# Kernel optimization log

Measured on AMD Instinct MI355X. Metric: run time of the kernel, lower is better.

Reference implementation:

```python
import jax, jax.numpy as jnp
import numpy as np

B, D = 8192, 1024
HR, HE, HF = 512, 4096, 2048
N_OPS, N_TASKS = 4, 4

def setup_inputs() -> dict:
    key = jax.random.key(0)
    ks = jax.random.split(key, 20)
    s = 0.02
    return {
        "x":        jax.random.normal(ks[0], (B, D), jnp.float32),
        # router
        "W_r1":   s*jax.random.normal(ks[1], (D, HR), jnp.float32),
        "b_r1":     jnp.zeros((HR,), jnp.float32),
        "W_dom":  s*jax.random.normal(ks[2], (HR, 2), jnp.float32),
        "b_dom":    jnp.zeros((2,), jnp.float32),
        "W_mop":  s*jax.random.normal(ks[3], (HR, N_OPS), jnp.float32),
        "W_lt":   s*jax.random.normal(ks[4], (HR, N_TASKS), jnp.float32),
        # math expert (operation hint = additive embedding)
        "op_emb": s*jax.random.normal(ks[5], (N_OPS, D), jnp.float32),
        "W_m1":   s*jax.random.normal(ks[6], (D, HE), jnp.float32),
        "b_m1":     jnp.zeros((HE,), jnp.float32),
        "W_m2":   s*jax.random.normal(ks[7], (HE, D), jnp.float32),
        "b_m2":     jnp.zeros((D,), jnp.float32),
        # language expert (task hint = additive embedding)
        "task_emb": s*jax.random.normal(ks[8], (N_TASKS, D), jnp.float32),
        "W_l1":   s*jax.random.normal(ks[9], (D, HE), jnp.float32),
        "b_l1":     jnp.zeros((HE,), jnp.float32),
        "W_l2":   s*jax.random.normal(ks[10], (HE, D), jnp.float32),
        "b_l2":     jnp.zeros((D,), jnp.float32),
        # fusion
        "W_f1":   s*jax.random.normal(ks[11], (D, HF), jnp.float32),
        "b_f1":     jnp.zeros((HF,), jnp.float32),
        "W_f2":   s*jax.random.normal(ks[12], (HF, D), jnp.float32),
        "b_f2":     jnp.zeros((D,), jnp.float32),
    }

def reference(x, W_r1, b_r1, W_dom, b_dom, W_mop, W_lt,
              op_emb, W_m1, b_m1, W_m2, b_m2,
              task_emb, W_l1, b_l1, W_l2, b_l2,
              W_f1, b_f1, W_f2, b_f2):
    # --- router ---
    h = jax.nn.relu(x @ W_r1 + b_r1)                      # [B, HR]
    dom_logits = h @ W_dom + b_dom                        # [B, 2]
    expert_weights = jax.nn.softmax(dom_logits, axis=-1)  # [B, 2]
    primary = jnp.argmax(dom_logits, axis=-1)             # [B]
    math_op = jnp.argmax(h @ W_mop, axis=-1)              # [B]
    lang_task = jnp.argmax(h @ W_lt, axis=-1)             # [B]
    # --- experts (vectorized equivalent of per-sample dispatch) ---
    math_in = x + op_emb[math_op]                         # [B, D]
    math_out = jax.nn.relu(math_in @ W_m1 + b_m1) @ W_m2 + b_m2
    lang_in = x + task_emb[lang_task]                     # [B, D]
    lang_out = jax.nn.relu(lang_in @ W_l1 + b_l1) @ W_l2 + b_l2
    selected = jnp.where((primary == 0)[:, None], math_out, lang_out)  # [B, D]
    # --- fusion: scale by routing weight of the chosen expert + MLP residual ---
    w = jnp.take_along_axis(expert_weights, primary[:, None], axis=1)  # [B, 1]
    fused = w * selected
    final = fused + jax.nn.relu(fused @ W_f1 + b_f1) @ W_f2 + b_f2     # [B, D]
    return final
```

## Files before the change

kernel.cpp:

```cpp
#include <hip/hip_runtime.h>
#include <hip/hip_bf16.h>
#include <stdint.h>

#define NB 8192
#define DD 1024
#define HRD 512
#define HED 4096
#define HFD 2048

typedef __attribute__((ext_vector_type(8))) short bf16x8;
typedef __attribute__((ext_vector_type(4))) float f32x4;
typedef unsigned short u16;

__device__ __forceinline__ u16 f2b(float f) {
    union { float f; uint32_t i; } c; c.f = f;
    uint32_t r = c.i + 0x7FFF + ((c.i >> 16) & 1);
    return (u16)(r >> 16);
}
__device__ __forceinline__ float b2f(u16 u) {
    union { uint32_t i; float f; } c; c.i = ((uint32_t)u) << 16; return c.f;
}

__global__ void k_init(int* cnt) { if (threadIdx.x < 2) cnt[threadIdx.x] = 0; }

__global__ __launch_bounds__(256) void k_split(const float4* __restrict__ x4,
                                               ushort4* __restrict__ hi4,
                                               ushort4* __restrict__ lo4) {
    int i = blockIdx.x * 256 + threadIdx.x;
    float4 v = x4[i];
    ushort4 h, l;
    h.x = f2b(v.x); l.x = f2b(v.x - b2f(h.x));
    h.y = f2b(v.y); l.y = f2b(v.y - b2f(h.y));
    h.z = f2b(v.z); l.z = f2b(v.z - b2f(h.z));
    h.w = f2b(v.w); l.w = f2b(v.w - b2f(h.w));
    hi4[i] = h; lo4[i] = l;
}

__global__ __launch_bounds__(256) void k_transpose(const float* __restrict__ in,
                                                   u16* __restrict__ out, int R, int C) {
    __shared__ float s[64][65];
    int tx = threadIdx.x & 63, ty = threadIdx.x >> 6;
    int c0 = blockIdx.x * 64, r0 = blockIdx.y * 64;
#pragma unroll
    for (int j = 0; j < 16; j++) { int r = ty + j * 4; s[r][tx] = in[(size_t)(r0 + r) * C + c0 + tx]; }
    __syncthreads();
#pragma unroll
    for (int j = 0; j < 16; j++) { int c = ty + j * 4; out[(size_t)(c0 + c) * R + r0 + tx] = f2b(s[tx][c]); }
}

__global__ __launch_bounds__(256) void k_transpose_split(const float* __restrict__ in,
                                                         u16* __restrict__ ohi, u16* __restrict__ olo,
                                                         int R, int C) {
    __shared__ float s[64][65];
    int tx = threadIdx.x & 63, ty = threadIdx.x >> 6;
    int c0 = blockIdx.x * 64, r0 = blockIdx.y * 64;
#pragma unroll
    for (int j = 0; j < 16; j++) { int r = ty + j * 4; s[r][tx] = in[(size_t)(r0 + r) * C + c0 + tx]; }
    __syncthreads();
#pragma unroll
    for (int j = 0; j < 16; j++) {
        int c = ty + j * 4;
        float v = s[tx][c];
        u16 h = f2b(v);
        ohi[(size_t)(c0 + c) * R + r0 + tx] = h;
        olo[(size_t)(c0 + c) * R + r0 + tx] = f2b(v - b2f(h));
    }
}

__device__ __forceinline__ void stage_tile(const char* gRowBase, long rowStrideBytes,
                                           int rowsClamp, u16* s, int tid) {
    int wave = tid >> 6, lane = tid & 63;
#pragma unroll
    for (int is = 0; is < 4; ++is) {
        int c = wave * 4 + is;
        int row = c * 8 + (lane >> 3);
        if (row > rowsClamp) row = rowsClamp;
        const char* g = gRowBase + (long)row * rowStrideBytes + (lane & 7) * 16;
        __builtin_amdgcn_global_load_lds(
            (const __attribute__((address_space(1))) void*)g,
            (__attribute__((address_space(3))) void*)((char*)s + c * 1024),
            16, 0, 0);
    }
}

__global__ __launch_bounds__(256) void k_router(const u16* __restrict__ Ah, const u16* __restrict__ Al,
                                                const u16* __restrict__ Bh, const u16* __restrict__ Bl,
                                                const float* __restrict__ bias, float* __restrict__ H) {
    __shared__ u16 sAh[128 * 64], sAl[128 * 64], sBh[128 * 64], sBl[128 * 64];
    int tid = threadIdx.x, lane = tid & 63, wave = tid >> 6;
    int bn = blockIdx.x, bm = blockIdx.y;
    f32x4 acc[4][4];
#pragma unroll
    for (int i = 0; i < 4; i++)
#pragma unroll
        for (int j = 0; j < 4; j++) acc[i][j] = (f32x4)0.f;
    int wm = (wave & 1) * 64, wn = (wave >> 1) * 64;
    for (int k0 = 0; k0 < DD; k0 += 64) {
        stage_tile((const char*)(Ah + (size_t)bm * 128 * DD + k0), DD * 2, 127, sAh, tid);
        stage_tile((const char*)(Al + (size_t)bm * 128 * DD + k0), DD * 2, 127, sAl, tid);
        stage_tile((const char*)(Bh + (size_t)bn * 128 * DD + k0), DD * 2, 127, sBh, tid);
        stage_tile((const char*)(Bl + (size_t)bn * 128 * DD + k0), DD * 2, 127, sBl, tid);
        __syncthreads();
#pragma unroll
        for (int kk = 0; kk < 2; kk++) {
            int kofs = kk * 64 + (lane >> 4) * 16;
            bf16x8 vbh[4], vbl[4];
#pragma unroll
            for (int ni = 0; ni < 4; ni++) {
                int rB = (wn + ni * 16 + (lane & 15)) * 128 + kofs;
                vbh[ni] = *(const bf16x8*)((const char*)sBh + rB);
                vbl[ni] = *(const bf16x8*)((const char*)sBl + rB);
            }
#pragma unroll
            for (int mi = 0; mi < 4; mi++) {
                int rA = (wm + mi * 16 + (lane & 15)) * 128 + kofs;
                bf16x8 vah = *(const bf16x8*)((const char*)sAh + rA);
                bf16x8 val = *(const bf16x8*)((const char*)sAl + rA);
#pragma unroll
                for (int ni = 0; ni < 4; ni++) {
                    acc[mi][ni] = __builtin_amdgcn_mfma_f32_16x16x32_bf16(vah, vbh[ni], acc[mi][ni], 0, 0, 0);
                    acc[mi][ni] = __builtin_amdgcn_mfma_f32_16x16x32_bf16(vah, vbl[ni], acc[mi][ni], 0, 0, 0);
                    acc[mi][ni] = __builtin_amdgcn_mfma_f32_16x16x32_bf16(val, vbh[ni], acc[mi][ni], 0, 0, 0);
                }
            }
        }
        __syncthreads();
    }
    int quad = lane >> 4, cl = lane & 15;
#pragma unroll
    for (int mi = 0; mi < 4; mi++)
#pragma unroll
        for (int r = 0; r < 4; r++) {
            int row = bm * 128 + wm + mi * 16 + quad * 4 + r;
#pragma unroll
            for (int ni = 0; ni < 4; ni++) {
                int col = bn * 128 + wn + ni * 16 + cl;
                float v = acc[mi][ni][r] + bias[col];
                H[(size_t)row * HRD + col] = fmaxf(v, 0.f);
            }
        }
}

__global__ __launch_bounds__(256) void k_heads(const float* __restrict__ H,
                                               const float* __restrict__ Wd, const float* __restrict__ bd,
                                               const float* __restrict__ Wm, const float* __restrict__ Wl,
                                               int* __restrict__ cnt, int* __restrict__ perm,
                                               float* __restrict__ wsc, int* __restrict__ eic) {
    int lane = threadIdx.x & 63, wave = threadIdx.x >> 6;
    int r = blockIdx.x * 4 + wave;
    const float4* h4 = (const float4*)(H + (size_t)r * HRD);
    float4 v0 = h4[lane * 2], v1 = h4[lane * 2 + 1];
    float hv[8] = {v0.x, v0.y, v0.z, v0.w, v1.x, v1.y, v1.z, v1.w};
    float a[10];
#pragma unroll
    for (int t = 0; t < 10; t++) a[t] = 0.f;
    int kbase = lane * 8;
#pragma unroll
    for (int j = 0; j < 8; j++) {
        int k = kbase + j;
        float h_ = hv[j];
        float2 wd = ((const float2*)Wd)[k];
        a[0] += h_ * wd.x; a[1] += h_ * wd.y;
        float4 wm = ((const float4*)Wm)[k];
        a[2] += h_ * wm.x; a[3] += h_ * wm.y; a[4] += h_ * wm.z; a[5] += h_ * wm.w;
        float4 wl = ((const float4*)Wl)[k];
        a[6] += h_ * wl.x; a[7] += h_ * wl.y; a[8] += h_ * wl.z; a[9] += h_ * wl.w;
    }
#pragma unroll
    for (int t = 0; t < 10; t++)
#pragma unroll
        for (int off = 32; off > 0; off >>= 1) a[t] += __shfl_down(a[t], off);
    if (lane == 0) {
        float d0 = a[0] + bd[0], d1 = a[1] + bd[1];
        int primary = (d1 > d0) ? 1 : 0;
        float w = 1.f / (1.f + expf(-fabsf(d0 - d1)));
        int mi = 0; float mv = a[2];
        if (a[3] > mv) { mv = a[3]; mi = 1; }
        if (a[4] > mv) { mv = a[4]; mi = 2; }
        if (a[5] > mv) { mv = a[5]; mi = 3; }
        int li = 0; float lv = a[6];
        if (a[7] > lv) { lv = a[7]; li = 1; }
        if (a[8] > lv) { lv = a[8]; li = 2; }
        if (a[9] > lv) { lv = a[9]; li = 3; }
        int pos;
        if (primary == 0) pos = atomicAdd(&cnt[0], 1);
        else              pos = NB - 1 - atomicAdd(&cnt[1], 1);
        perm[pos] = r; wsc[pos] = w; eic[pos] = (primary == 0) ? mi : li;
    }
}

__global__ __launch_bounds__(256) void k_gather(const float* __restrict__ x,
                                                const float* __restrict__ op_emb,
                                                const float* __restrict__ task_emb,
                                                const int* __restrict__ perm, const int* __restrict__ eic,
                                                const int* __restrict__ cnt, u16* __restrict__ xin) {
    int lane = threadIdx.x & 63, wave = threadIdx.x >> 6;
    int i = blockIdx.x * 4 + wave;
    int n0 = cnt[0];
    int r = perm[i];
    const float* emb = ((i >= n0) ? task_emb : op_emb) + (size_t)eic[i] * DD;
    const float4* x4 = (const float4*)(x + (size_t)r * DD);
    const float4* e4 = (const float4*)emb;
    ushort4* o4 = (ushort4*)(xin + (size_t)i * DD);
#pragma unroll
    for (int j = 0; j < 4; j++) {
        int idx = lane + j * 64;
        float4 xv = x4[idx], ev = e4[idx];
        ushort4 o;
        o.x = f2b(xv.x + ev.x); o.y = f2b(xv.y + ev.y);
        o.z = f2b(xv.z + ev.z); o.w = f2b(xv.w + ev.w);
        o4[idx] = o;
    }
}

template <int EPI>
__global__ __launch_bounds__(256) void k_gemm_bt(const u16* __restrict__ A, const u16* __restrict__ Bt,
                                                 const float* __restrict__ bias, void* __restrict__ Out,
                                                 int K, int N, const int* __restrict__ cnt, int expertSel,
                                                 const float* __restrict__ wsel, const int* __restrict__ perm,
                                                 const u16* __restrict__ resid) {
    __shared__ u16 sA[128 * 64];
    __shared__ u16 sB[128 * 64];
    int tid = threadIdx.x, lane = tid & 63, wave = tid >> 6;
    int bn = blockIdx.x, bm = blockIdx.y;
    int rowStart = 0, rowCount = NB;
    if (expertSel == 0) { rowCount = cnt[0]; }
    else if (expertSel == 1) { rowStart = cnt[0]; rowCount = NB - rowStart; }
    if (bm * 128 >= rowCount) return;
    int rcA = rowCount - bm * 128 - 1; if (rcA > 127) rcA = 127;
    f32x4 acc[4][4];
#pragma unroll
    for (int i = 0; i < 4; i++)
#pragma unroll
        for (int j = 0; j < 4; j++) acc[i][j] = (f32x4)0.f;
    int wm = (wave & 1) * 64, wn = (wave >> 1) * 64;
    const char* aBase = (const char*)(A + (size_t)(rowStart + bm * 128) * K);
    const char* bBase = (const char*)(Bt + (size_t)bn * 128 * K);
    for (int k0 = 0; k0 < K; k0 += 64) {
        stage_tile(aBase + (size_t)k0 * 2, (long)K * 2, rcA, sA, tid);
        stage_tile(bBase + (size_t)k0 * 2, (long)K * 2, 127, sB, tid);
        __syncthreads();
#pragma unroll
        for (int kk = 0; kk < 2; kk++) {
            int kofs = kk * 64 + (lane >> 4) * 16;
            bf16x8 vb[4];
#pragma unroll
            for (int ni = 0; ni < 4; ni++)
                vb[ni] = *(const bf16x8*)((const char*)sB + (wn + ni * 16 + (lane & 15)) * 128 + kofs);
#pragma unroll
            for (int mi = 0; mi < 4; mi++) {
                bf16x8 va = *(const bf16x8*)((const char*)sA + (wm + mi * 16 + (lane & 15)) * 128 + kofs);
#pragma unroll
                for (int ni = 0; ni < 4; ni++)
                    acc[mi][ni] = __builtin_amdgcn_mfma_f32_16x16x32_bf16(va, vb[ni], acc[mi][ni], 0, 0, 0);
            }
        }
        __syncthreads();
    }
    int quad = lane >> 4, cl = lane & 15;
#pragma unroll
    for (int mi = 0; mi < 4; mi++)
#pragma unroll
        for (int r = 0; r < 4; r++) {
            int lrow = bm * 128 + wm + mi * 16 + quad * 4 + r;
            if (lrow >= rowCount) continue;
            int grow = rowStart + lrow;
#pragma unroll
            for (int ni = 0; ni < 4; ni++) {
                int col = bn * 128 + wn + ni * 16 + cl;
                float v = acc[mi][ni][r] + bias[col];
                if constexpr (EPI == 0) {
                    ((u16*)Out)[(size_t)grow * N + col] = f2b(fmaxf(v, 0.f));
                } else if constexpr (EPI == 1) {
                    ((u16*)Out)[(size_t)grow * N + col] = f2b(v * wsel[grow]);
                } else {
                    v += b2f(resid[(size_t)grow * N + col]);
                    ((float*)Out)[(size_t)perm[grow] * N + col] = v;
                }
            }
        }
}

extern "C" void kernel_launch(void* const* d_in, const int* in_sizes, int n_in,
                              void* d_out, int out_size, void* d_ws, size_t ws_size,
                              hipStream_t stream) {
    const float* x      = (const float*)d_in[0];
    const float* W_r1   = (const float*)d_in[1];
    const float* b_r1   = (const float*)d_in[2];
    const float* W_dom  = (const float*)d_in[3];
    const float* b_dom  = (const float*)d_in[4];
    const float* W_mop  = (const float*)d_in[5];
    const float* W_lt   = (const float*)d_in[6];
    const float* op_emb = (const float*)d_in[7];
    const float* W_m1   = (const float*)d_in[8];
    const float* b_m1   = (const float*)d_in[9];
    const float* W_m2   = (const float*)d_in[10];
    const float* b_m2   = (const float*)d_in[11];
    const float* task_emb = (const float*)d_in[12];
    const float* W_l1   = (const float*)d_in[13];
    const float* b_l1   = (const float*)d_in[14];
    const float* W_l2   = (const float*)d_in[15];
    const float* b_l2   = (const float*)d_in[16];
    const float* W_f1   = (const float*)d_in[17];
    const float* b_f1   = (const float*)d_in[18];
    const float* W_f2   = (const float*)d_in[19];
    const float* b_f2   = (const float*)d_in[20];

    char* wsp = (char*)d_ws;
    size_t off = 0;
    auto take = [&](size_t bytes) -> char* {
        char* p = wsp + off;
        off += (bytes + 255) & ~(size_t)255;
        return p;
    };
    u16* Wr_hi = (u16*)take((size_t)HRD * DD * 2);
    u16* Wr_lo = (u16*)take((size_t)HRD * DD * 2);
    u16* Wm1t  = (u16*)take((size_t)HED * DD * 2);
    u16* Wl1t  = (u16*)take((size_t)HED * DD * 2);
    u16* Wm2t  = (u16*)take((size_t)DD * HED * 2);
    u16* Wl2t  = (u16*)take((size_t)DD * HED * 2);
    u16* Wf1t  = (u16*)take((size_t)HFD * DD * 2);
    u16* Wf2t  = (u16*)take((size_t)DD * HFD * 2);
    u16* x_hi  = (u16*)take((size_t)NB * DD * 2);
    u16* x_lo  = (u16*)take((size_t)NB * DD * 2);
    float* Hbuf = (float*)take((size_t)NB * HRD * 4);
    u16* hid   = (u16*)take((size_t)NB * HED * 2);
    int* cnt   = (int*)take(256);
    int* perm  = (int*)take(NB * 4);
    int* eic   = (int*)take(NB * 4);
    float* wsc = (float*)take(NB * 4);
    u16* xin   = x_hi;
    u16* fused = x_lo;
    u16* hid2  = Wm1t;

    k_init<<<1, 64, 0, stream>>>(cnt);
    k_split<<<(NB * DD / 4) / 256, 256, 0, stream>>>((const float4*)x, (ushort4*)x_hi, (ushort4*)x_lo);
    k_transpose_split<<<dim3(HRD / 64, DD / 64), 256, 0, stream>>>(W_r1, Wr_hi, Wr_lo, DD, HRD);
    k_transpose<<<dim3(HED / 64, DD / 64), 256, 0, stream>>>(W_m1, Wm1t, DD, HED);
    k_transpose<<<dim3(HED / 64, DD / 64), 256, 0, stream>>>(W_l1, Wl1t, DD, HED);
    k_transpose<<<dim3(DD / 64, HED / 64), 256, 0, stream>>>(W_m2, Wm2t, HED, DD);
    k_transpose<<<dim3(DD / 64, HED / 64), 256, 0, stream>>>(W_l2, Wl2t, HED, DD);
    k_transpose<<<dim3(HFD / 64, DD / 64), 256, 0, stream>>>(W_f1, Wf1t, DD, HFD);
    k_transpose<<<dim3(DD / 64, HFD / 64), 256, 0, stream>>>(W_f2, Wf2t, HFD, DD);

    k_router<<<dim3(HRD / 128, NB / 128), 256, 0, stream>>>(x_hi, x_lo, Wr_hi, Wr_lo, b_r1, Hbuf);
    k_heads<<<NB / 4, 256, 0, stream>>>(Hbuf, W_dom, b_dom, W_mop, W_lt, cnt, perm, wsc, eic);
    k_gather<<<NB / 4, 256, 0, stream>>>(x, op_emb, task_emb, perm, eic, cnt, xin);

    k_gemm_bt<0><<<dim3(HED / 128, NB / 128), 256, 0, stream>>>(xin, Wm1t, b_m1, hid, DD, HED, cnt, 0, nullptr, nullptr, nullptr);
    k_gemm_bt<0><<<dim3(HED / 128, NB / 128), 256, 0, stream>>>(xin, Wl1t, b_l1, hid, DD, HED, cnt, 1, nullptr, nullptr, nullptr);
    k_gemm_bt<1><<<dim3(DD / 128, NB / 128), 256, 0, stream>>>(hid, Wm2t, b_m2, fused, HED, DD, cnt, 0, wsc, nullptr, nullptr);
    k_gemm_bt<1><<<dim3(DD / 128, NB / 128), 256, 0, stream>>>(hid, Wl2t, b_l2, fused, HED, DD, cnt, 1, wsc, nullptr, nullptr);
    k_gemm_bt<0><<<dim3(HFD / 128, NB / 128), 256, 0, stream>>>(fused, Wf1t, b_f1, hid2, DD, HFD, cnt, -1, nullptr, nullptr, nullptr);
    k_gemm_bt<2><<<dim3(DD / 128, NB / 128), 256, 0, stream>>>(hid2, Wf2t, b_f2, d_out, HFD, DD, cnt, -1, nullptr, perm, fused);
}
```

Before: 791.8 us.

## Merge math and language expert GEMMs into single dual-expert launches

The separate math and language expert GEMM launches are replaced with one combined kernel per layer. It covers 65 row tiles and chooses the weight matrix per tile, so the boundary tile is computed twice and each copy stores only its own rows. This removes the mostly-empty launches and the tail imbalance from splitting the grid per expert. The grid order is also switched to put the M dimension fastest in some GEMMs and the router, and the row-clamp in tile staging is removed. Without the clamp, the last tile may read past the valid rows of its buffer.

```diff
diff --git a/kernel.cpp b/kernel.cpp
--- a/kernel.cpp
+++ b/kernel.cpp
@@ -68,13 +68,12 @@
 }
 
 __device__ __forceinline__ void stage_tile(const char* gRowBase, long rowStrideBytes,
-                                           int rowsClamp, u16* s, int tid) {
+                                           u16* s, int tid) {
     int wave = tid >> 6, lane = tid & 63;
 #pragma unroll
     for (int is = 0; is < 4; ++is) {
         int c = wave * 4 + is;
         int row = c * 8 + (lane >> 3);
-        if (row > rowsClamp) row = rowsClamp;
         const char* g = gRowBase + (long)row * rowStrideBytes + (lane & 7) * 16;
         __builtin_amdgcn_global_load_lds(
             (const __attribute__((address_space(1))) void*)g,
@@ -88,7 +87,7 @@
                                                 const float* __restrict__ bias, float* __restrict__ H) {
     __shared__ u16 sAh[128 * 64], sAl[128 * 64], sBh[128 * 64], sBl[128 * 64];
     int tid = threadIdx.x, lane = tid & 63, wave = tid >> 6;
-    int bn = blockIdx.x, bm = blockIdx.y;
+    int bm = blockIdx.x, bn = blockIdx.y;
     f32x4 acc[4][4];
 #pragma unroll
     for (int i = 0; i < 4; i++)
@@ -96,10 +95,10 @@
         for (int j = 0; j < 4; j++) acc[i][j] = (f32x4)0.f;
     int wm = (wave & 1) * 64, wn = (wave >> 1) * 64;
     for (int k0 = 0; k0 < DD; k0 += 64) {
-        stage_tile((const char*)(Ah + (size_t)bm * 128 * DD + k0), DD * 2, 127, sAh, tid);
-        stage_tile((const char*)(Al + (size_t)bm * 128 * DD + k0), DD * 2, 127, sAl, tid);
-        stage_tile((const char*)(Bh + (size_t)bn * 128 * DD + k0), DD * 2, 127, sBh, tid);
-        stage_tile((const char*)(Bl + (size_t)bn * 128 * DD + k0), DD * 2, 127, sBl, tid);
+        stage_tile((const char*)(Ah + (size_t)bm * 128 * DD + k0), DD * 2, sAh, tid);
+        stage_tile((const char*)(Al + (size_t)bm * 128 * DD + k0), DD * 2, sAl, tid);
+        stage_tile((const char*)(Bh + (size_t)bn * 128 * DD + k0), DD * 2, sBh, tid);
+        stage_tile((const char*)(Bl + (size_t)bn * 128 * DD + k0), DD * 2, sBl, tid);
         __syncthreads();
 #pragma unroll
         for (int kk = 0; kk < 2; kk++) {
@@ -181,8 +180,8 @@
         int li = 0; float lv = a[6];
         if (a[7] > lv) { lv = a[7]; li = 1; }
         if (a[8] > lv) { lv = a[8]; li = 2; }
+        int pos;
         if (a[9] > lv) { lv = a[9]; li = 3; }
-        int pos;
         if (primary == 0) pos = atomicAdd(&cnt[0], 1);
         else              pos = NB - 1 - atomicAdd(&cnt[1], 1);
         perm[pos] = r; wsc[pos] = w; eic[pos] = (primary == 0) ? mi : li;
@@ -213,32 +212,38 @@
     }
 }
 
-template <int EPI>
-__global__ __launch_bounds__(256) void k_gemm_bt(const u16* __restrict__ A, const u16* __restrict__ Bt,
-                                                 const float* __restrict__ bias, void* __restrict__ Out,
-                                                 int K, int N, const int* __restrict__ cnt, int expertSel,
-                                                 const float* __restrict__ wsel, const int* __restrict__ perm,
-                                                 const u16* __restrict__ resid) {
+template <int EPI, bool BMFAST>
+__global__ __launch_bounds__(256) void k_gemm_dual(const u16* __restrict__ A,
+                                                   const u16* __restrict__ Btm, const u16* __restrict__ Btl,
+                                                   const float* __restrict__ biasm, const float* __restrict__ biasl,
+                                                   u16* __restrict__ Out, int K, int N,
+                                                   const int* __restrict__ cnt, const float* __restrict__ wsel) {
     __shared__ u16 sA[128 * 64];
     __shared__ u16 sB[128 * 64];
     int tid = threadIdx.x, lane = tid & 63, wave = tid >> 6;
-    int bn = blockIdx.x, bm = blockIdx.y;
-    int rowStart = 0, rowCount = NB;
-    if (expertSel == 0) { rowCount = cnt[0]; }
-    else if (expertSel == 1) { rowStart = cnt[0]; rowCount = NB - rowStart; }
-    if (bm * 128 >= rowCount) return;
-    int rcA = rowCount - bm * 128 - 1; if (rcA > 127) rcA = 127;
+    int bn, t;
+    if (BMFAST) { t = blockIdx.x; bn = blockIdx.y; } else { bn = blockIdx.x; t = blockIdx.y; }
+    int n0 = cnt[0];
+    int tb = n0 >> 7;
+    bool isMath = (t <= tb) && (t < 64);
+    int tile = isMath ? t : (t - 1);
+    int storeLo, storeHi;
+    if (isMath) { storeLo = tile * 128; storeHi = n0 < storeLo + 128 ? n0 : storeLo + 128; }
+    else        { storeHi = tile * 128 + 128; storeLo = n0 > tile * 128 ? n0 : tile * 128; }
+    if (storeLo >= storeHi) return;
+    const u16* Bt = isMath ? Btm : Btl;
+    const float* bias = isMath ? biasm : biasl;
     f32x4 acc[4][4];
 #pragma unroll
     for (int i = 0; i < 4; i++)
 #pragma unroll
         for (int j = 0; j < 4; j++) acc[i][j] = (f32x4)0.f;
     int wm = (wave & 1) * 64, wn = (wave >> 1) * 64;
-    const char* aBase = (const char*)(A + (size_t)(rowStart + bm * 128) * K);
+    const char* aBase = (const char*)(A + (size_t)tile * 128 * K);
     const char* bBase = (const char*)(Bt + (size_t)bn * 128 * K);
     for (int k0 = 0; k0 < K; k0 += 64) {
-        stage_tile(aBase + (size_t)k0 * 2, (long)K * 2, rcA, sA, tid);
-        stage_tile(bBase + (size_t)k0 * 2, (long)K * 2, 127, sB, tid);
+        stage_tile(aBase + (size_t)k0 * 2, (long)K * 2, sA, tid);
+        stage_tile(bBase + (size_t)k0 * 2, (long)K * 2, sB, tid);
         __syncthreads();
 #pragma unroll
         for (int kk = 0; kk < 2; kk++) {
@@ -262,17 +267,72 @@
     for (int mi = 0; mi < 4; mi++)
 #pragma unroll
         for (int r = 0; r < 4; r++) {
-            int lrow = bm * 128 + wm + mi * 16 + quad * 4 + r;
-            if (lrow >= rowCount) continue;
-            int grow = rowStart + lrow;
+            int grow = tile * 128 + wm + mi * 16 + quad * 4 + r;
+            if (grow < storeLo || grow >= storeHi) continue;
+#pragma unroll
+            for (int ni = 0; ni < 4; ni++) {
+                int col = bn * 128 + wn + ni * 16 + cl;
+                float v = acc[mi][ni][r] + bias[col];
+                if constexpr (EPI == 0) {
+                    Out[(size_t)grow * N + col] = f2b(fmaxf(v, 0.f));
+                } else {
+                    Out[(size_t)grow * N + col] = f2b(v * wsel[grow]);
+                }
+            }
+        }
+}
+
+template <int EPI, bool BMFAST>
+__global__ __launch_bounds__(256) void k_gemm_bt(const u16* __restrict__ A, const u16* __restrict__ Bt,
+                                                 const float* __restrict__ bias, void* __restrict__ Out,
+                                                 int K, int N,
+                                                 const int* __restrict__ perm, const u16* __restrict__ resid) {
+    __shared__ u16 sA[128 * 64];
+    __shared__ u16 sB[128 * 64];
+    int tid = threadIdx.x, lane = tid & 63, wave = tid >> 6;
+    int bn, bm;
+    if (BMFAST) { bm = blockIdx.x; bn = blockIdx.y; } else { bn = blockIdx.x; bm = blockIdx.y; }
+    f32x4 acc[4][4];
+#pragma unroll
+    for (int i = 0; i < 4; i++)
+#pragma unroll
+        for (int j = 0; j < 4; j++) acc[i][j] = (f32x4)0.f;
+    int wm = (wave & 1) * 64, wn = (wave >> 1) * 64;
+    const char* aBase = (const char*)(A + (size_t)bm * 128 * K);
+    const char* bBase = (const char*)(Bt + (size_t)bn * 128 * K);
+    for (int k0 = 0; k0 < K; k0 += 64) {
+        stage_tile(aBase + (size_t)k0 * 2, (long)K * 2, sA, tid);
+        stage_tile(bBase + (size_t)k0 * 2, (long)K * 2, sB, tid);
+        __syncthreads();
+#pragma unroll
+        for (int kk = 0; kk < 2; kk++) {
+            int kofs = kk * 64 + (lane >> 4) * 16;
+            bf16x8 vb[4];
+#pragma unroll
+            for (int ni = 0; ni < 4; ni++)
+                vb[ni] = *(const bf16x8*)((const char*)sB + (wn + ni * 16 + (lane & 15)) * 128 + kofs);
+#pragma unroll
+            for (int mi = 0; mi < 4; mi++) {
+                bf16x8 va = *(const bf16x8*)((const char*)sA + (wm + mi * 16 + (lane & 15)) * 128 + kofs);
+#pragma unroll
+                for (int ni = 0; ni < 4; ni++)
+                    acc[mi][ni] = __builtin_amdgcn_mfma_f32_16x16x32_bf16(va, vb[ni], acc[mi][ni], 0, 0, 0);
+            }
+        }
+        __syncthreads();
+    }
+    int quad = lane >> 4, cl = lane & 15;
+#pragma unroll
+    for (int mi = 0; mi < 4; mi++)
+#pragma unroll
+        for (int r = 0; r < 4; r++) {
+            int grow = bm * 128 + wm + mi * 16 + quad * 4 + r;
 #pragma unroll
             for (int ni = 0; ni < 4; ni++) {
                 int col = bn * 128 + wn + ni * 16 + cl;
                 float v = acc[mi][ni][r] + bias[col];
                 if constexpr (EPI == 0) {
                     ((u16*)Out)[(size_t)grow * N + col] = f2b(fmaxf(v, 0.f));
-                } else if constexpr (EPI == 1) {
-                    ((u16*)Out)[(size_t)grow * N + col] = f2b(v * wsel[grow]);
                 } else {
                     v += b2f(resid[(size_t)grow * N + col]);
                     ((float*)Out)[(size_t)perm[grow] * N + col] = v;
@@ -343,14 +403,16 @@
     k_transpose<<<dim3(HFD / 64, DD / 64), 256, 0, stream>>>(W_f1, Wf1t, DD, HFD);
     k_transpose<<<dim3(DD / 64, HFD / 64), 256, 0, stream>>>(W_f2, Wf2t, HFD, DD);
 
-    k_router<<<dim3(HRD / 128, NB / 128), 256, 0, stream>>>(x_hi, x_lo, Wr_hi, Wr_lo, b_r1, Hbuf);
+    k_router<<<dim3(NB / 128, HRD / 128), 256, 0, stream>>>(x_hi, x_lo, Wr_hi, Wr_lo, b_r1, Hbuf);
     k_heads<<<NB / 4, 256, 0, stream>>>(Hbuf, W_dom, b_dom, W_mop, W_lt, cnt, perm, wsc, eic);
     k_gather<<<NB / 4, 256, 0, stream>>>(x, op_emb, task_emb, perm, eic, cnt, xin);
 
-    k_gemm_bt<0><<<dim3(HED / 128, NB / 128), 256, 0, stream>>>(xin, Wm1t, b_m1, hid, DD, HED, cnt, 0, nullptr, nullptr, nullptr);
-    k_gemm_bt<0><<<dim3(HED / 128, NB / 128), 256, 0, stream>>>(xin, Wl1t, b_l1, hid, DD, HED, cnt, 1, nullptr, nullptr, nullptr);
-    k_gemm_bt<1><<<dim3(DD / 128, NB / 128), 256, 0, stream>>>(hid, Wm2t, b_m2, fused, HED, DD, cnt, 0, wsc, nullptr, nullptr);
-    k_gemm_bt<1><<<dim3(DD / 128, NB / 128), 256, 0, stream>>>(hid, Wl2t, b_l2, fused, HED, DD, cnt, 1, wsc, nullptr, nullptr);
-    k_gemm_bt<0><<<dim3(HFD / 128, NB / 128), 256, 0, stream>>>(fused, Wf1t, b_f1, hid2, DD, HFD, cnt, -1, nullptr, nullptr, nullptr);
-    k_gemm_bt<2><<<dim3(DD / 128, NB / 128), 256, 0, stream>>>(hid2, Wf2t, b_f2, d_out, HFD, DD, cnt, -1, nullptr, perm, fused);
-}
+    k_gemm_dual<0, false><<<dim3(HED / 128, NB / 128 + 1), 256, 0, stream>>>(
+        xin, Wm1t, Wl1t, b_m1, b_l1, hid, DD, HED, cnt, nullptr);
+    k_gemm_dual<1, true><<<dim3(NB / 128 + 1, DD / 128), 256, 0, stream>>>(
+        hid, Wm2t, Wl2t, b_m2, b_l2, fused, HED, DD, cnt, wsc);
+    k_gemm_bt<0, false><<<dim3(HFD / 128, NB / 128), 256, 0, stream>>>(
+        fused, Wf1t, b_f1, hid2, DD, HFD, nullptr, nullptr);
+    k_gemm_bt<2, true><<<dim3(NB / 128, DD / 128), 256, 0, stream>>>(
+        hid2, Wf2t, b_f2, d_out, HFD, DD, perm, fused);
+}
```

Measured after the change: 757.0 us. -4.4%, faster.

## Merge per-expert GEMMs into one dual-expert launch with 64x256 tiles

Applied to the files above, without the earlier changes.

Replaces the separate math and language expert GEMM launches with a single dual-expert kernel. Each 64-row tile picks its expert weights by comparing the tile's rows against the math/language split count, so the boundary tile is computed twice and each copy stores only its own rows. GEMM tiles change from 128x128 to 64x256, with each wave owning a 64x64 block, and the router GEMM moves to 64x128 tiles with a reordered grid. The aim is to cut launch count and idle or early-exit blocks, keep the grid size fixed regardless of routing, and improve B-operand reuse. The cost is less A-tile reuse per block and more LDS traffic for the wider B tile.

```diff
diff --git a/kernel.cpp b/kernel.cpp
--- a/kernel.cpp
+++ b/kernel.cpp
@@ -19,6 +19,10 @@
 }
 __device__ __forceinline__ float b2f(u16 u) {
     union { uint32_t i; float f; } c; c.i = ((uint32_t)u) << 16; return c.f;
+}
+__device__ __forceinline__ void glds16(const char* g, char* l) {
+    __builtin_amdgcn_global_load_lds((const __attribute__((address_space(1))) void*)g,
+                                     (__attribute__((address_space(3))) void*)l, 16, 0, 0);
 }
 
 __global__ void k_init(int* cnt) { if (threadIdx.x < 2) cnt[threadIdx.x] = 0; }
@@ -67,39 +71,38 @@
     }
 }
 
-__device__ __forceinline__ void stage_tile(const char* gRowBase, long rowStrideBytes,
-                                           int rowsClamp, u16* s, int tid) {
-    int wave = tid >> 6, lane = tid & 63;
-#pragma unroll
-    for (int is = 0; is < 4; ++is) {
-        int c = wave * 4 + is;
-        int row = c * 8 + (lane >> 3);
-        if (row > rowsClamp) row = rowsClamp;
-        const char* g = gRowBase + (long)row * rowStrideBytes + (lane & 7) * 16;
-        __builtin_amdgcn_global_load_lds(
-            (const __attribute__((address_space(1))) void*)g,
-            (__attribute__((address_space(3))) void*)((char*)s + c * 1024),
-            16, 0, 0);
-    }
-}
-
 __global__ __launch_bounds__(256) void k_router(const u16* __restrict__ Ah, const u16* __restrict__ Al,
                                                 const u16* __restrict__ Bh, const u16* __restrict__ Bl,
                                                 const float* __restrict__ bias, float* __restrict__ H) {
-    __shared__ u16 sAh[128 * 64], sAl[128 * 64], sBh[128 * 64], sBl[128 * 64];
+    __shared__ u16 sAh[64 * 64], sAl[64 * 64], sBh[128 * 64], sBl[128 * 64];
     int tid = threadIdx.x, lane = tid & 63, wave = tid >> 6;
-    int bn = blockIdx.x, bm = blockIdx.y;
-    f32x4 acc[4][4];
-#pragma unroll
-    for (int i = 0; i < 4; i++)
+    int bm = blockIdx.x, bn = blockIdx.y;
+    f32x4 acc[2][4];
+#pragma unroll
+    for (int i = 0; i < 2; i++)
 #pragma unroll
         for (int j = 0; j < 4; j++) acc[i][j] = (f32x4)0.f;
-    int wm = (wave & 1) * 64, wn = (wave >> 1) * 64;
+    int wm = (wave & 1) * 32, wn = (wave >> 1) * 64;
+    const long ks = DD * 2;
+    const char* ahB = (const char*)Ah + (size_t)bm * 64 * ks;
+    const char* alB = (const char*)Al + (size_t)bm * 64 * ks;
+    const char* bhB = (const char*)Bh + (size_t)bn * 128 * ks;
+    const char* blB = (const char*)Bl + (size_t)bn * 128 * ks;
     for (int k0 = 0; k0 < DD; k0 += 64) {
-        stage_tile((const char*)(Ah + (size_t)bm * 128 * DD + k0), DD * 2, 127, sAh, tid);
-        stage_tile((const char*)(Al + (size_t)bm * 128 * DD + k0), DD * 2, 127, sAl, tid);
-        stage_tile((const char*)(Bh + (size_t)bn * 128 * DD + k0), DD * 2, 127, sBh, tid);
-        stage_tile((const char*)(Bl + (size_t)bn * 128 * DD + k0), DD * 2, 127, sBl, tid);
+#pragma unroll
+        for (int is = 0; is < 2; is++) {
+            int c = wave * 2 + is;
+            long go = (long)(c * 8 + (lane >> 3)) * ks + k0 * 2 + (lane & 7) * 16;
+            glds16(ahB + go, (char*)sAh + c * 1024);
+            glds16(alB + go, (char*)sAl + c * 1024);
+        }
+#pragma unroll
+        for (int is = 0; is < 4; is++) {
+            int c = wave * 4 + is;
+            long go = (long)(c * 8 + (lane >> 3)) * ks + k0 * 2 + (lane & 7) * 16;
+            glds16(bhB + go, (char*)sBh + c * 1024);
+            glds16(blB + go, (char*)sBl + c * 1024);
+        }
         __syncthreads();
 #pragma unroll
         for (int kk = 0; kk < 2; kk++) {
@@ -112,7 +115,7 @@
                 vbl[ni] = *(const bf16x8*)((const char*)sBl + rB);
             }
 #pragma unroll
-            for (int mi = 0; mi < 4; mi++) {
+            for (int mi = 0; mi < 2; mi++) {
                 int rA = (wm + mi * 16 + (lane & 15)) * 128 + kofs;
                 bf16x8 vah = *(const bf16x8*)((const char*)sAh + rA);
                 bf16x8 val = *(const bf16x8*)((const char*)sAl + rA);
@@ -128,10 +131,10 @@
     }
     int quad = lane >> 4, cl = lane & 15;
 #pragma unroll
-    for (int mi = 0; mi < 4; mi++)
+    for (int mi = 0; mi < 2; mi++)
 #pragma unroll
         for (int r = 0; r < 4; r++) {
-            int row = bm * 128 + wm + mi * 16 + quad * 4 + r;
+            int row = bm * 64 + wm + mi * 16 + quad * 4 + r;
 #pragma unroll
             for (int ni = 0; ni < 4; ni++) {
                 int col = bn * 128 + wn + ni * 16 + cl;
@@ -213,32 +216,54 @@
     }
 }
 
-template <int EPI>
-__global__ __launch_bounds__(256) void k_gemm_bt(const u16* __restrict__ A, const u16* __restrict__ Bt,
-                                                 const float* __restrict__ bias, void* __restrict__ Out,
-                                                 int K, int N, const int* __restrict__ cnt, int expertSel,
-                                                 const float* __restrict__ wsel, const int* __restrict__ perm,
-                                                 const u16* __restrict__ resid) {
-    __shared__ u16 sA[128 * 64];
-    __shared__ u16 sB[128 * 64];
+template <int EPI, bool DUAL>
+__global__ __launch_bounds__(256) void k_gemm64(const u16* __restrict__ A,
+                                                const u16* __restrict__ Btm, const u16* __restrict__ Btl,
+                                                const float* __restrict__ biasm, const float* __restrict__ biasl,
+                                                void* __restrict__ Out, int K, int N,
+                                                const int* __restrict__ cnt, const float* __restrict__ wsel,
+                                                const int* __restrict__ perm, const u16* __restrict__ resid) {
+    __shared__ u16 sA[64 * 64];
+    __shared__ u16 sB[256 * 64];
     int tid = threadIdx.x, lane = tid & 63, wave = tid >> 6;
-    int bn = blockIdx.x, bm = blockIdx.y;
-    int rowStart = 0, rowCount = NB;
-    if (expertSel == 0) { rowCount = cnt[0]; }
-    else if (expertSel == 1) { rowStart = cnt[0]; rowCount = NB - rowStart; }
-    if (bm * 128 >= rowCount) return;
-    int rcA = rowCount - bm * 128 - 1; if (rcA > 127) rcA = 127;
+    int t = blockIdx.x, bn = blockIdx.y;
+    int tile = t, storeLo, storeHi;
+    const u16* Bt = Btm; const float* bias = biasm;
+    if constexpr (DUAL) {
+        int n0 = cnt[0];
+        int tb = n0 >> 6;
+        bool isMath = (t <= tb) && (t < NB / 64);
+        tile = isMath ? t : t - 1;
+        int lo = tile * 64, hi = lo + 64;
+        if (isMath) { storeLo = lo; storeHi = n0 < hi ? n0 : hi; }
+        else        { storeLo = n0 > lo ? n0 : lo; storeHi = hi; }
+        if (storeLo >= storeHi) return;
+        if (!isMath) { Bt = Btl; bias = biasl; }
+    } else {
+        storeLo = t * 64; storeHi = storeLo + 64;
+    }
     f32x4 acc[4][4];
 #pragma unroll
     for (int i = 0; i < 4; i++)
 #pragma unroll
         for (int j = 0; j < 4; j++) acc[i][j] = (f32x4)0.f;
-    int wm = (wave & 1) * 64, wn = (wave >> 1) * 64;
-    const char* aBase = (const char*)(A + (size_t)(rowStart + bm * 128) * K);
-    const char* bBase = (const char*)(Bt + (size_t)bn * 128 * K);
+    int wn = wave * 64;
+    const long ks = (long)K * 2;
+    const char* aBase = (const char*)A + (size_t)tile * 64 * ks;
+    const char* bBase = (const char*)Bt + (size_t)bn * 256 * ks;
     for (int k0 = 0; k0 < K; k0 += 64) {
-        stage_tile(aBase + (size_t)k0 * 2, (long)K * 2, rcA, sA, tid);
-        stage_tile(bBase + (size_t)k0 * 2, (long)K * 2, 127, sB, tid);
+#pragma unroll
+        for (int is = 0; is < 2; is++) {
+            int c = wave * 2 + is;
+            long go = (long)(c * 8 + (lane >> 3)) * ks + k0 * 2 + (lane & 7) * 16;
+            glds16(aBase + go, (char*)sA + c * 1024);
+        }
+#pragma unroll
+        for (int is = 0; is < 8; is++) {
+            int c = wave * 8 + is;
+            long go = (long)(c * 8 + (lane >> 3)) * ks + k0 * 2 + (lane & 7) * 16;
+            glds16(bBase + go, (char*)sB + c * 1024);
+        }
         __syncthreads();
 #pragma unroll
         for (int kk = 0; kk < 2; kk++) {
@@ -249,7 +274,7 @@
                 vb[ni] = *(const bf16x8*)((const char*)sB + (wn + ni * 16 + (lane & 15)) * 128 + kofs);
 #pragma unroll
             for (int mi = 0; mi < 4; mi++) {
-                bf16x8 va = *(const bf16x8*)((const char*)sA + (wm + mi * 16 + (lane & 15)) * 128 + kofs);
+                bf16x8 va = *(const bf16x8*)((const char*)sA + (mi * 16 + (lane & 15)) * 128 + kofs);
 #pragma unroll
                 for (int ni = 0; ni < 4; ni++)
                     acc[mi][ni] = __builtin_amdgcn_mfma_f32_16x16x32_bf16(va, vb[ni], acc[mi][ni], 0, 0, 0);
@@ -262,17 +287,18 @@
     for (int mi = 0; mi < 4; mi++)
 #pragma unroll
         for (int r = 0; r < 4; r++) {
-            int lrow = bm * 128 + wm + mi * 16 + quad * 4 + r;
-            if (lrow >= rowCount) continue;
-            int grow = rowStart + lrow;
+            int grow = tile * 64 + mi * 16 + quad * 4 + r;
+            if (grow < storeLo || grow >= storeHi) continue;
+            float wrow = 0.f;
+            if constexpr (EPI == 1) wrow = wsel[grow];
 #pragma unroll
             for (int ni = 0; ni < 4; ni++) {
-                int col = bn * 128 + wn + ni * 16 + cl;
+                int col = bn * 256 + wn + ni * 16 + cl;
                 float v = acc[mi][ni][r] + bias[col];
                 if constexpr (EPI == 0) {
                     ((u16*)Out)[(size_t)grow * N + col] = f2b(fmaxf(v, 0.f));
                 } else if constexpr (EPI == 1) {
-                    ((u16*)Out)[(size_t)grow * N + col] = f2b(v * wsel[grow]);
+                    ((u16*)Out)[(size_t)grow * N + col] = f2b(v * wrow);
                 } else {
                     v += b2f(resid[(size_t)grow * N + col]);
                     ((float*)Out)[(size_t)perm[grow] * N + col] = v;
@@ -343,14 +369,16 @@
     k_transpose<<<dim3(HFD / 64, DD / 64), 256, 0, stream>>>(W_f1, Wf1t, DD, HFD);
     k_transpose<<<dim3(DD / 64, HFD / 64), 256, 0, stream>>>(W_f2, Wf2t, HFD, DD);
 
-    k_router<<<dim3(HRD / 128, NB / 128), 256, 0, stream>>>(x_hi, x_lo, Wr_hi, Wr_lo, b_r1, Hbuf);
+    k_router<<<dim3(NB / 64, HRD / 128), 256, 0, stream>>>(x_hi, x_lo, Wr_hi, Wr_lo, b_r1, Hbuf);
     k_heads<<<NB / 4, 256, 0, stream>>>(Hbuf, W_dom, b_dom, W_mop, W_lt, cnt, perm, wsc, eic);
     k_gather<<<NB / 4, 256, 0, stream>>>(x, op_emb, task_emb, perm, eic, cnt, xin);
 
-    k_gemm_bt<0><<<dim3(HED / 128, NB / 128), 256, 0, stream>>>(xin, Wm1t, b_m1, hid, DD, HED, cnt, 0, nullptr, nullptr, nullptr);
-    k_gemm_bt<0><<<dim3(HED / 128, NB / 128), 256, 0, stream>>>(xin, Wl1t, b_l1, hid, DD, HED, cnt, 1, nullptr, nullptr, nullptr);
-    k_gemm_bt<1><<<dim3(DD / 128, NB / 128), 256, 0, stream>>>(hid, Wm2t, b_m2, fused, HED, DD, cnt, 0, wsc, nullptr, nullptr);
-    k_gemm_bt<1><<<dim3(DD / 128, NB / 128), 256, 0, stream>>>(hid, Wl2t, b_l2, fused, HED, DD, cnt, 1, wsc, nullptr, nullptr);
-    k_gemm_bt<0><<<dim3(HFD / 128, NB / 128), 256, 0, stream>>>(fused, Wf1t, b_f1, hid2, DD, HFD, cnt, -1, nullptr, nullptr, nullptr);
-    k_gemm_bt<2><<<dim3(DD / 128, NB / 128), 256, 0, stream>>>(hid2, Wf2t, b_f2, d_out, HFD, DD, cnt, -1, nullptr, perm, fused);
-}
+    k_gemm64<0, true><<<dim3(NB / 64 + 1, HED / 256), 256, 0, stream>>>(
+        xin, Wm1t, Wl1t, b_m1, b_l1, hid, DD, HED, cnt, nullptr, nullptr, nullptr);
+    k_gemm64<1, true><<<dim3(NB / 64 + 1, DD / 256), 256, 0, stream>>>(
+        hid, Wm2t, Wl2t, b_m2, b_l2, fused, HED, DD, cnt, wsc, nullptr, nullptr);
+    k_gemm64<0, false><<<dim3(NB / 64, HFD / 256), 256, 0, stream>>>(
+        fused, Wf1t, nullptr, b_f1, nullptr, hid2, DD, HFD, nullptr, nullptr, nullptr, nullptr);
+    k_gemm64<2, false><<<dim3(NB / 64, DD / 256), 256, 0, stream>>>(
+        hid2, Wf2t, nullptr, b_f2, nullptr, d_out, HFD, DD, nullptr, nullptr, perm, fused);
+}
```

New measurement: 771.4 us. 1.03x faster.
